# Optimization experiments

Measured on AMD Instinct MI355X. Metric: run time of the kernel, lower is better.

Reference implementation:

```python
import jax, jax.numpy as jnp
import numpy as np

H = 16          # local heads
DN = 128        # qk_nope_head_dim
DR = 64         # qk_rope_head_dim
DV = 128        # v_head_dim
QL = 1536       # q_lora_rank
KVL = 512       # kv_lora_rank
HID = 5120      # hidden_size
T = 2048        # tokens
EPS = 1e-6
THETA = 10000.0
SCALE = (DN + DR) ** -0.5


def rmsnorm(x, w):
    return x * jax.lax.rsqrt(jnp.mean(x * x, axis=-1, keepdims=True) + EPS) * w


def rope_interleaved(x, pos):
    # non-neox (GPT-J interleaved) partial RoPE on last dim DR; x: [T, h, DR]
    inv_freq = 1.0 / (THETA ** (jnp.arange(0, DR, 2, dtype=jnp.float32) / DR))
    freqs = pos[:, None].astype(jnp.float32) * inv_freq          # [T, DR/2]
    cos = jnp.cos(freqs)[:, None, :]
    sin = jnp.sin(freqs)[:, None, :]
    x1, x2 = x[..., 0::2], x[..., 1::2]
    o1 = x1 * cos - x2 * sin
    o2 = x2 * cos + x1 * sin
    return jnp.stack([o1, o2], axis=-1).reshape(x.shape)


def setup_inputs() -> dict:
    key = jax.random.key(0)
    ks = jax.random.split(key, 8)
    s = lambda d: 1.0 / np.sqrt(d)
    return {
        "positions": jnp.arange(T, dtype=jnp.int64),
        "hidden_states": jax.random.normal(ks[0], (T, HID), jnp.float32),
        "wq_a": jax.random.normal(ks[1], (HID, QL), jnp.float32) * s(HID),
        "q_a_ln": jnp.ones((QL,), jnp.float32),
        "wq_b": jax.random.normal(ks[2], (QL, H * (DN + DR)), jnp.float32) * s(QL),
        "wkv_a": jax.random.normal(ks[3], (HID, KVL + DR), jnp.float32) * s(HID),
        "kv_a_ln": jnp.ones((KVL,), jnp.float32),
        "wkv_b": jax.random.normal(ks[4], (KVL, H * (DN + DV)), jnp.float32) * s(KVL),
        "wo": jax.random.normal(ks[5], (H * DV, HID), jnp.float32) * s(H * DV),
    }


def reference(positions, hidden_states, wq_a, q_a_ln, wq_b, wkv_a, kv_a_ln, wkv_b, wo):
    Tn = hidden_states.shape[0]
    # Q path: low-rank down, RMSNorm, up to per-head qk dims
    q = rmsnorm(hidden_states @ wq_a, q_a_ln) @ wq_b            # [T, H*(DN+DR)]
    q = q.reshape(Tn, H, DN + DR)
    q_nope, q_pe = q[..., :DN], q[..., DN:]
    # KV path: joint down-projection -> latent + shared rope key
    kv = hidden_states @ wkv_a                                   # [T, KVL+DR]
    c_kv, k_pe = kv[:, :KVL], kv[:, KVL:]
    c_kv = rmsnorm(c_kv, kv_a_ln)
    kvb = (c_kv @ wkv_b).reshape(Tn, H, DN + DV)
    k_nope, v = kvb[..., :DN], kvb[..., DN:]
    # partial RoPE on rope sub-dims only
    q_pe = rope_interleaved(q_pe, positions)                     # [T, H, DR]
    k_pe = rope_interleaved(k_pe[:, None, :], positions)         # [T, 1, DR]
    # causal attention over full qk_head_dim
    scores = (jnp.einsum('thd,shd->hts', q_nope, k_nope)
              + jnp.einsum('thd,sod->hts', q_pe, k_pe)) * SCALE  # [H, T, T]
    mask = jnp.tril(jnp.ones((Tn, Tn), bool))
    scores = jnp.where(mask[None], scores, jnp.finfo(scores.dtype).min)
    attn = jax.nn.softmax(scores, axis=-1)
    out = jnp.einsum('hts,shd->thd', attn, v).reshape(Tn, H * DV)
    return out @ wo                                              # [T, HID]
```

## Files before the change

kernel.cpp:

```cpp
#include <hip/hip_runtime.h>
#include <hip/hip_bf16.h>

typedef __attribute__((ext_vector_type(8))) short bf16x8;
typedef __attribute__((ext_vector_type(4))) short bf16x4;
typedef __attribute__((ext_vector_type(4))) float f32x4;

typedef __attribute__((address_space(1))) const unsigned int gu32;
typedef __attribute__((address_space(3))) unsigned int lu32;

#define ATTN_SCALE 0.07216878364870323f

static __device__ __forceinline__ float bf2f(__hip_bfloat16 b) { return __bfloat162float(b); }

__global__ void cvt_kernel(const float* __restrict__ in, __hip_bfloat16* __restrict__ out, int n) {
  for (int i = (blockIdx.x * 256 + threadIdx.x) * 4; i < n; i += gridDim.x * 256 * 4) {
    float4 v = *(const float4*)(in + i);
    out[i + 0] = __float2bfloat16(v.x);
    out[i + 1] = __float2bfloat16(v.y);
    out[i + 2] = __float2bfloat16(v.z);
    out[i + 3] = __float2bfloat16(v.w);
  }
}

__global__ void transpose_cvt_kernel(const float* __restrict__ in, __hip_bfloat16* __restrict__ out,
                                     int R, int C) {
  __shared__ float tile[32][33];
  int bi = blockIdx.x, bj = blockIdx.y;
  int tx = threadIdx.x & 31, ty = threadIdx.x >> 5;
#pragma unroll
  for (int k2 = 0; k2 < 4; k2++) {
    int r = bi * 32 + ty + k2 * 8;
    tile[ty + k2 * 8][tx] = in[(size_t)r * C + bj * 32 + tx];
  }
  __syncthreads();
#pragma unroll
  for (int k2 = 0; k2 < 4; k2++) {
    int cc = bj * 32 + ty + k2 * 8;
    out[(size_t)cc * R + bi * 32 + tx] = __float2bfloat16(tile[tx][ty + k2 * 8]);
  }
}

__global__ void rmsnorm_kernel(const float* __restrict__ in, int in_stride, int cols,
                               const float* __restrict__ wgt,
                               __hip_bfloat16* __restrict__ out, int out_stride) {
  int row = blockIdx.x;
  const float* x = in + (size_t)row * in_stride;
  float ss = 0.f;
  for (int c = threadIdx.x; c < cols; c += 256) { float v = x[c]; ss += v * v; }
#pragma unroll
  for (int d = 1; d < 64; d <<= 1) ss += __shfl_xor(ss, d, 64);
  __shared__ float red[4];
  if ((threadIdx.x & 63) == 0) red[threadIdx.x >> 6] = ss;
  __syncthreads();
  float tot = red[0] + red[1] + red[2] + red[3];
  float r = rsqrtf(tot / cols + 1e-6f);
  __hip_bfloat16* o = out + (size_t)row * out_stride;
  for (int c = threadIdx.x; c < cols; c += 256)
    o[c] = __float2bfloat16(x[c] * r * wgt[c]);
}

__global__ void rope_q_kernel(__hip_bfloat16* __restrict__ q) {
  int row = blockIdx.x;
#pragma unroll
  for (int jj = 0; jj < 2; jj++) {
    int v = threadIdx.x + 256 * jj;
    int h = v >> 5, i = v & 31;
    float inv = powf(10000.f, -(2.f * i) / 64.f);
    float fr = (float)row * inv;
    float s, c;
    sincosf(fr, &s, &c);
    __hip_bfloat16* p = q + (size_t)row * 3072 + h * 192 + 128 + 2 * i;
    float x1 = bf2f(p[0]), x2 = bf2f(p[1]);
    p[0] = __float2bfloat16(x1 * c - x2 * s);
    p[1] = __float2bfloat16(x2 * c + x1 * s);
  }
}

__global__ void rope_k_kernel(const float* __restrict__ src, int stride,
                              __hip_bfloat16* __restrict__ kpe) {
  int row = blockIdx.x;
  int i = threadIdx.x;
  if (i < 32) {
    float inv = powf(10000.f, -(2.f * i) / 64.f);
    float fr = (float)row * inv;
    float s, c;
    sincosf(fr, &s, &c);
    float x1 = src[(size_t)row * stride + 2 * i];
    float x2 = src[(size_t)row * stride + 2 * i + 1];
    kpe[(size_t)row * 64 + 2 * i]     = __float2bfloat16(x1 * c - x2 * s);
    kpe[(size_t)row * 64 + 2 * i + 1] = __float2bfloat16(x2 * c + x1 * s);
  }
}

template <int MODE>
__global__ __launch_bounds__(256, 2) void gemm_lds_kernel(
    const __hip_bfloat16* __restrict__ A, const __hip_bfloat16* __restrict__ Bt,
    void* __restrict__ Cout, __hip_bfloat16* __restrict__ KnopeOut,
    __hip_bfloat16* __restrict__ VtOut, int M, int N, int K) {
  __shared__ __hip_bfloat16 As[2][128][32];
  __shared__ __hip_bfloat16 Bs[2][128][32];
  const int t = threadIdx.x;
  const int w = t >> 6, l = t & 63;
  const int lr = l & 15, lh = l >> 4;
  const int wr = w >> 1, wc = w & 1;
  const int bm = blockIdx.x, bn = blockIdx.y;

  const int r0 = l >> 2;
  const int c0 = (l & 3) * 8;
  const int rowA0 = w * 16 + r0;
  const int rowA1 = (4 + w) * 16 + r0;
  const __hip_bfloat16* Ag0 = A + (size_t)(bm * 128 + rowA0) * K + c0;
  const __hip_bfloat16* Ag1 = A + (size_t)(bm * 128 + rowA1) * K + c0;
  int br0 = bn * 128 + rowA0; if (br0 >= N) br0 = N - 1;
  int br1 = bn * 128 + rowA1; if (br1 >= N) br1 = N - 1;
  const __hip_bfloat16* Bg0 = Bt + (size_t)br0 * K + c0;
  const __hip_bfloat16* Bg1 = Bt + (size_t)br1 * K + c0;

  f32x4 acc[4][4];
#pragma unroll
  for (int i = 0; i < 4; i++)
#pragma unroll
    for (int j = 0; j < 4; j++) acc[i][j] = f32x4{0.f, 0.f, 0.f, 0.f};

  auto issue = [&](int kt, int buf) {
    const int ko = kt * 32;
    __builtin_amdgcn_global_load_lds((gu32*)(Ag0 + ko), (lu32*)&As[buf][rowA0][c0], 16, 0, 0);
    __builtin_amdgcn_global_load_lds((gu32*)(Ag1 + ko), (lu32*)&As[buf][rowA1][c0], 16, 0, 0);
    __builtin_amdgcn_global_load_lds((gu32*)(Bg0 + ko), (lu32*)&Bs[buf][rowA0][c0], 16, 0, 0);
    __builtin_amdgcn_global_load_lds((gu32*)(Bg1 + ko), (lu32*)&Bs[buf][rowA1][c0], 16, 0, 0);
  };

  const int KT = K >> 5;
  issue(0, 0);
  int cur = 0;
  for (int kt = 0; kt < KT; ++kt) {
    __syncthreads();
    if (kt + 1 < KT) issue(kt + 1, cur ^ 1);
    bf16x8 af[4], bff[4];
#pragma unroll
    for (int m = 0; m < 4; m++) af[m] = *(bf16x8*)&As[cur][wr * 64 + m * 16 + lr][lh * 8];
#pragma unroll
    for (int n = 0; n < 4; n++) bff[n] = *(bf16x8*)&Bs[cur][wc * 64 + n * 16 + lr][lh * 8];
    __builtin_amdgcn_s_setprio(1);
#pragma unroll
    for (int m = 0; m < 4; m++)
#pragma unroll
      for (int n = 0; n < 4; n++)
        acc[m][n] = __builtin_amdgcn_mfma_f32_16x16x32_bf16(af[m], bff[n], acc[m][n], 0, 0, 0);
    __builtin_amdgcn_s_setprio(0);
    cur ^= 1;
  }
#pragma unroll
  for (int m = 0; m < 4; m++) {
    int row = bm * 128 + wr * 64 + m * 16 + lh * 4;
#pragma unroll
    for (int n = 0; n < 4; n++) {
      int col = bn * 128 + wc * 64 + n * 16 + lr;
      if (MODE == 2) {
        int hcol = ((col >> 8) << 7) + (col & 127);
        if ((bn & 1) == 0) {
#pragma unroll
          for (int j = 0; j < 4; j++)
            KnopeOut[(size_t)(row + j) * 2048 + hcol] = __float2bfloat16(acc[m][n][j]);
        } else {
          bf16x4 pk;
#pragma unroll
          for (int j = 0; j < 4; j++) {
            union { __hip_bfloat16 b; short s; } cv;
            cv.b = __float2bfloat16(acc[m][n][j]);
            pk[j] = cv.s;
          }
          *(bf16x4*)(VtOut + (size_t)hcol * 2048 + row) = pk;
        }
      } else if (col < N) {
#pragma unroll
        for (int j = 0; j < 4; j++) {
          if (MODE == 1)
            ((__hip_bfloat16*)Cout)[(size_t)(row + j) * N + col] = __float2bfloat16(acc[m][n][j]);
          else
            ((float*)Cout)[(size_t)(row + j) * N + col] = acc[m][n][j];
        }
      }
    }
  }
}

__global__ __launch_bounds__(256, 2) void attn_kernel(
    const __hip_bfloat16* __restrict__ Q, const __hip_bfloat16* __restrict__ Knope,
    const __hip_bfloat16* __restrict__ Vt, const __hip_bfloat16* __restrict__ KPE,
    __hip_bfloat16* __restrict__ Out) {
  __shared__ __hip_bfloat16 Ks[64][200];
  __shared__ __hip_bfloat16 Vs[128][72];
  __shared__ __hip_bfloat16 Ps[4][16][72];

  const int t = threadIdx.x;
  const int w = t >> 6, l = t & 63;
  const int lr = l & 15, lh = l >> 4;
  const int bm = (int)gridDim.x - 1 - (int)blockIdx.x;
  const int h = blockIdx.y;

  bf16x8 aq[6];
  {
    const int qrow = bm * 64 + w * 16 + lr;
    const __hip_bfloat16* qp = Q + (size_t)qrow * 3072 + h * 192 + lh * 8;
#pragma unroll
    for (int ks = 0; ks < 6; ks++) aq[ks] = *(const bf16x8*)(qp + ks * 32);
  }

  f32x4 o_acc[8];
#pragma unroll
  for (int i = 0; i < 8; i++) o_acc[i] = f32x4{0.f, 0.f, 0.f, 0.f};
  float m_run[4], l_run[4];
#pragma unroll
  for (int j = 0; j < 4; j++) { m_run[j] = -INFINITY; l_run[j] = 0.f; }

  bf16x8 kreg[6], vreg[4];
  auto load_regs = [&](int kb) {
    const int s0 = kb * 64;
#pragma unroll
    for (int j = 0; j < 6; j++) {
      int c = t + 256 * j;
      int row = c / 24, col8 = (c % 24) * 8;
      const __hip_bfloat16* src = (col8 < 128)
          ? Knope + (size_t)(s0 + row) * 2048 + h * 128 + col8
          : KPE + (size_t)(s0 + row) * 64 + (col8 - 128);
      kreg[j] = *(const bf16x8*)src;
    }
#pragma unroll
    for (int j = 0; j < 4; j++) {
      int c = t + 256 * j;
      int dv = c >> 3;
      int sc = c & 7;
      vreg[j] = *(const bf16x8*)(Vt + (size_t)(h * 128 + dv) * 2048 + s0 + sc * 8);
    }
  };
  auto store_tile = [&]() {
#pragma unroll
    for (int j = 0; j < 6; j++) {
      int c = t + 256 * j;
      int row = c / 24, col8 = (c % 24) * 8;
      *(bf16x8*)&Ks[row][col8] = kreg[j];
    }
#pragma unroll
    for (int j = 0; j < 4; j++) {
      int c = t + 256 * j;
      int dv = c >> 3, sc = c & 7;
      *(bf16x8*)&Vs[dv][(sc ^ ((dv >> 3) & 7)) << 3] = vreg[j];
    }
  };

  load_regs(0);
  for (int kb = 0; kb <= bm; ++kb) {
    const int s0 = kb * 64;
    store_tile();
    __syncthreads();
    if (kb < bm) load_regs(kb + 1);

    f32x4 sa[4];
#pragma unroll
    for (int nf = 0; nf < 4; nf++) sa[nf] = f32x4{0.f, 0.f, 0.f, 0.f};
#pragma unroll
    for (int ks = 0; ks < 6; ks++) {
#pragma unroll
      for (int nf = 0; nf < 4; nf++) {
        bf16x8 b = *(bf16x8*)&Ks[nf * 16 + lr][ks * 32 + lh * 8];
        sa[nf] = __builtin_amdgcn_mfma_f32_16x16x32_bf16(aq[ks], b, sa[nf], 0, 0, 0);
      }
    }
    float sv[4][4];
    const bool diag = (kb == bm);
#pragma unroll
    for (int nf = 0; nf < 4; nf++) {
      int scol = s0 + nf * 16 + lr;
#pragma unroll
      for (int j = 0; j < 4; j++) {
        float x = sa[nf][j] * ATTN_SCALE;
        if (diag) {
          int qr = bm * 64 + w * 16 + lh * 4 + j;
          if (scol > qr) x = -1e30f;
        }
        sv[nf][j] = x;
      }
    }
    float pm[4], fac[4];
#pragma unroll
    for (int j = 0; j < 4; j++) {
      float mx = fmaxf(fmaxf(sv[0][j], sv[1][j]), fmaxf(sv[2][j], sv[3][j]));
#pragma unroll
      for (int d = 1; d < 16; d <<= 1) mx = fmaxf(mx, __shfl_xor(mx, d, 64));
      float mn = fmaxf(m_run[j], mx);
      fac[j] = __expf(m_run[j] - mn);
      m_run[j] = mn;
      pm[j] = mn;
    }
    float rs[4] = {0.f, 0.f, 0.f, 0.f};
#pragma unroll
    for (int nf = 0; nf < 4; nf++) {
#pragma unroll
      for (int j = 0; j < 4; j++) {
        float p = __expf(sv[nf][j] - pm[j]);
        rs[j] += p;
        Ps[w][lh * 4 + j][nf * 16 + lr] = __float2bfloat16(p);
      }
    }
#pragma unroll
    for (int j = 0; j < 4; j++) {
      float s = rs[j];
#pragma unroll
      for (int d = 1; d < 16; d <<= 1) s += __shfl_xor(s, d, 64);
      l_run[j] = l_run[j] * fac[j] + s;
    }
#pragma unroll
    for (int nf = 0; nf < 8; nf++)
#pragma unroll
      for (int j = 0; j < 4; j++) o_acc[nf][j] *= fac[j];

#pragma unroll
    for (int ks = 0; ks < 2; ks++) {
      bf16x8 pa = *(bf16x8*)&Ps[w][lr][ks * 32 + lh * 8];
#pragma unroll
      for (int nf = 0; nf < 8; nf++) {
        int dv = nf * 16 + lr;
        int c8 = ks * 4 + lh;
        bf16x8 vb = *(bf16x8*)&Vs[dv][((c8 ^ ((dv >> 3) & 7)) << 3)];
        o_acc[nf] = __builtin_amdgcn_mfma_f32_16x16x32_bf16(pa, vb, o_acc[nf], 0, 0, 0);
      }
    }
    __syncthreads();
  }
#pragma unroll
  for (int nf = 0; nf < 8; nf++) {
    int col = h * 128 + nf * 16 + lr;
#pragma unroll
    for (int j = 0; j < 4; j++) {
      int row = bm * 64 + w * 16 + lh * 4 + j;
      Out[(size_t)row * 2048 + col] = __float2bfloat16(o_acc[nf][j] / l_run[j]);
    }
  }
}

extern "C" void kernel_launch(void* const* d_in, const int* in_sizes, int n_in,
                              void* d_out, int out_size, void* d_ws, size_t ws_size,
                              hipStream_t stream) {
  const float* hidden  = (const float*)d_in[1];
  const float* wq_a    = (const float*)d_in[2];
  const float* q_a_ln  = (const float*)d_in[3];
  const float* wq_b    = (const float*)d_in[4];
  const float* wkv_a   = (const float*)d_in[5];
  const float* kv_a_ln = (const float*)d_in[6];
  const float* wkv_b   = (const float*)d_in[7];
  const float* wo      = (const float*)d_in[8];
  float* out = (float*)d_out;

  char* ws = (char*)d_ws;
  size_t off = 0;
  auto alloc = [&](size_t bytes) { void* p = ws + off; off += (bytes + 255) & ~(size_t)255; return p; };
  __hip_bfloat16* h_bf     = (__hip_bfloat16*)alloc((size_t)2048 * 5120 * 2);
  __hip_bfloat16* qkvw_t   = (__hip_bfloat16*)alloc((size_t)2112 * 5120 * 2);
  __hip_bfloat16* wq_b_t   = (__hip_bfloat16*)alloc((size_t)3072 * 1536 * 2);
  __hip_bfloat16* wkv_b_t  = (__hip_bfloat16*)alloc((size_t)4096 * 512 * 2);
  __hip_bfloat16* wo_t     = (__hip_bfloat16*)alloc((size_t)5120 * 2048 * 2);
  float*          qkv_lat  = (float*)alloc((size_t)2048 * 2112 * 4);
  __hip_bfloat16* q_a_bf   = (__hip_bfloat16*)alloc((size_t)2048 * 1536 * 2);
  __hip_bfloat16* ckv_bf   = (__hip_bfloat16*)alloc((size_t)2048 * 512 * 2);
  __hip_bfloat16* kpe_bf   = (__hip_bfloat16*)alloc((size_t)2048 * 64 * 2);
  __hip_bfloat16* q_bf     = (__hip_bfloat16*)alloc((size_t)2048 * 3072 * 2);
  __hip_bfloat16* knope_bf = (__hip_bfloat16*)alloc((size_t)2048 * 2048 * 2);
  __hip_bfloat16* vt_bf    = (__hip_bfloat16*)alloc((size_t)2048 * 2048 * 2);
  __hip_bfloat16* attn_o   = (__hip_bfloat16*)alloc((size_t)2048 * 2048 * 2);
  (void)ws_size; (void)in_sizes; (void)n_in; (void)out_size;

  cvt_kernel<<<1024, 256, 0, stream>>>(hidden, h_bf, 2048 * 5120);
  transpose_cvt_kernel<<<dim3(160, 48), 256, 0, stream>>>(wq_a, qkvw_t, 5120, 1536);
  transpose_cvt_kernel<<<dim3(160, 18), 256, 0, stream>>>(wkv_a, qkvw_t + (size_t)1536 * 5120, 5120, 576);
  transpose_cvt_kernel<<<dim3(48, 96), 256, 0, stream>>>(wq_b, wq_b_t, 1536, 3072);
  transpose_cvt_kernel<<<dim3(16, 128), 256, 0, stream>>>(wkv_b, wkv_b_t, 512, 4096);
  transpose_cvt_kernel<<<dim3(64, 160), 256, 0, stream>>>(wo, wo_t, 2048, 5120);

  gemm_lds_kernel<0><<<dim3(16, 17), 256, 0, stream>>>(h_bf, qkvw_t, qkv_lat, nullptr, nullptr,
                                                       2048, 2112, 5120);

  rmsnorm_kernel<<<2048, 256, 0, stream>>>(qkv_lat, 2112, 1536, q_a_ln, q_a_bf, 1536);
  rmsnorm_kernel<<<2048, 256, 0, stream>>>(qkv_lat + 1536, 2112, 512, kv_a_ln, ckv_bf, 512);
  rope_k_kernel<<<2048, 64, 0, stream>>>(qkv_lat + 2048, 2112, kpe_bf);

  gemm_lds_kernel<1><<<dim3(16, 24), 256, 0, stream>>>(q_a_bf, wq_b_t, q_bf, nullptr, nullptr,
                                                       2048, 3072, 1536);
  rope_q_kernel<<<2048, 256, 0, stream>>>(q_bf);

  gemm_lds_kernel<2><<<dim3(16, 32), 256, 0, stream>>>(ckv_bf, wkv_b_t, nullptr, knope_bf, vt_bf,
                                                       2048, 4096, 512);

  attn_kernel<<<dim3(32, 16), 256, 0, stream>>>(q_bf, knope_bf, vt_bf, kpe_bf, attn_o);

  gemm_lds_kernel<0><<<dim3(16, 40), 256, 0, stream>>>(attn_o, wo_t, out, nullptr, nullptr,
                                                       2048, 5120, 2048);
}
```

Measured before the change: 545.3 us.

## Split long causal attention rows into KV chunks with a combine kernel

The attention grid is split so that query blocks with long causal ranges process KV in chunks of 8 tiles across separate workgroups, producing 80x16 blocks instead of 32x16. Partial unnormalized outputs and running max/sum are written to a float workspace. A new combine kernel merges the partials with log-sum-exp rescaling. This aims to fix load imbalance and underuse of the GPU's compute units in causal attention, at the cost of extra global traffic for partials and one more kernel launch.

```diff
diff --git a/kernel.cpp b/kernel.cpp
--- a/kernel.cpp
+++ b/kernel.cpp
@@ -188,7 +188,7 @@
 __global__ __launch_bounds__(256, 2) void attn_kernel(
     const __hip_bfloat16* __restrict__ Q, const __hip_bfloat16* __restrict__ Knope,
     const __hip_bfloat16* __restrict__ Vt, const __hip_bfloat16* __restrict__ KPE,
-    __hip_bfloat16* __restrict__ Out) {
+    __hip_bfloat16* __restrict__ Out, float* __restrict__ Opart, float2* __restrict__ MLpart) {
   __shared__ __hip_bfloat16 Ks[64][200];
   __shared__ __hip_bfloat16 Vs[128][72];
   __shared__ __hip_bfloat16 Ps[4][16][72];
@@ -196,8 +196,18 @@
   const int t = threadIdx.x;
   const int w = t >> 6, l = t & 63;
   const int lr = l & 15, lh = l >> 4;
-  const int bm = (int)gridDim.x - 1 - (int)blockIdx.x;
   const int h = blockIdx.y;
+
+  const int x = blockIdx.x;
+  const int g = (x >= 48) ? 3 : (x >= 24) ? 2 : (x >= 8) ? 1 : 0;
+  const int Sg = (g == 3) ? 48 : (g == 2) ? 24 : (g == 1) ? 8 : 0;
+  const int r = x - Sg;
+  const int q = r / (g + 1);
+  const int bm = g * 8 + q;
+  const int ci = r - q * (g + 1);
+  const int kb0 = ci * 8;
+  const int kb_last = (bm < kb0 + 7) ? bm : kb0 + 7;
+  const bool partial = (g > 0);
 
   bf16x8 aq[6];
   {
@@ -249,12 +259,12 @@
     }
   };
 
-  load_regs(0);
-  for (int kb = 0; kb <= bm; ++kb) {
+  load_regs(kb0);
+  for (int kb = kb0; kb <= kb_last; ++kb) {
     const int s0 = kb * 64;
     store_tile();
     __syncthreads();
-    if (kb < bm) load_regs(kb + 1);
+    if (kb < kb_last) load_regs(kb + 1);
 
     f32x4 sa[4];
 #pragma unroll
@@ -274,12 +284,12 @@
       int scol = s0 + nf * 16 + lr;
 #pragma unroll
       for (int j = 0; j < 4; j++) {
-        float x = sa[nf][j] * ATTN_SCALE;
+        float xv = sa[nf][j] * ATTN_SCALE;
         if (diag) {
           int qr = bm * 64 + w * 16 + lh * 4 + j;
-          if (scol > qr) x = -1e30f;
+          if (scol > qr) xv = -1e30f;
         }
-        sv[nf][j] = x;
+        sv[nf][j] = xv;
       }
     }
     float pm[4], fac[4];
@@ -328,15 +338,78 @@
     }
     __syncthreads();
   }
-#pragma unroll
-  for (int nf = 0; nf < 8; nf++) {
-    int col = h * 128 + nf * 16 + lr;
-#pragma unroll
-    for (int j = 0; j < 4; j++) {
-      int row = bm * 64 + w * 16 + lh * 4 + j;
-      Out[(size_t)row * 2048 + col] = __float2bfloat16(o_acc[nf][j] / l_run[j]);
-    }
-  }
+
+  if (!partial) {
+#pragma unroll
+    for (int nf = 0; nf < 8; nf++) {
+      int col = h * 128 + nf * 16 + lr;
+#pragma unroll
+      for (int j = 0; j < 4; j++) {
+        int row = bm * 64 + w * 16 + lh * 4 + j;
+        Out[(size_t)row * 2048 + col] = __float2bfloat16(o_acc[nf][j] / l_run[j]);
+      }
+    }
+  } else {
+    const int base = ((g == 1) ? 0 : (g == 2) ? 16 : 40) + q * (g + 1);
+    const int slot = h * 72 + base + ci;
+    float* op = Opart + (size_t)slot * 8192;
+#pragma unroll
+    for (int nf = 0; nf < 8; nf++) {
+      int col = nf * 16 + lr;
+#pragma unroll
+      for (int j = 0; j < 4; j++) {
+        int row = w * 16 + lh * 4 + j;
+        op[row * 128 + col] = o_acc[nf][j];
+      }
+    }
+    if (lr == 0) {
+#pragma unroll
+      for (int j = 0; j < 4; j++) {
+        int row = w * 16 + lh * 4 + j;
+        MLpart[(size_t)slot * 64 + row] = float2{m_run[j], l_run[j]};
+      }
+    }
+  }
+}
+
+__global__ void attn_combine_kernel(const float* __restrict__ Opart,
+                                    const float2* __restrict__ MLpart,
+                                    __hip_bfloat16* __restrict__ Out) {
+  const int bm = 8 + blockIdx.x, h = blockIdx.y;
+  const int g = bm >> 3;
+  const int nch = g + 1;
+  const int base = ((g == 1) ? 0 : (g == 2) ? 16 : 40) + (bm & 7) * nch;
+  const int slot0 = h * 72 + base;
+  const int row = threadIdx.x >> 2;
+  const int c0 = (threadIdx.x & 3) * 32;
+
+  float M = -INFINITY;
+  for (int c = 0; c < nch; ++c) M = fmaxf(M, MLpart[(size_t)(slot0 + c) * 64 + row].x);
+  float L = 0.f;
+  for (int c = 0; c < nch; ++c) {
+    float2 ml = MLpart[(size_t)(slot0 + c) * 64 + row];
+    L += ml.y * __expf(ml.x - M);
+  }
+  float acc[32];
+#pragma unroll
+  for (int i = 0; i < 32; i++) acc[i] = 0.f;
+  for (int c = 0; c < nch; ++c) {
+    float2 ml = MLpart[(size_t)(slot0 + c) * 64 + row];
+    float sc = __expf(ml.x - M);
+    const float* op = Opart + (size_t)(slot0 + c) * 8192 + row * 128 + c0;
+#pragma unroll
+    for (int k = 0; k < 8; k++) {
+      float4 v = *(const float4*)(op + k * 4);
+      acc[k * 4 + 0] += sc * v.x;
+      acc[k * 4 + 1] += sc * v.y;
+      acc[k * 4 + 2] += sc * v.z;
+      acc[k * 4 + 3] += sc * v.w;
+    }
+  }
+  const float inv = 1.f / L;
+  __hip_bfloat16* o = Out + (size_t)(bm * 64 + row) * 2048 + h * 128 + c0;
+#pragma unroll
+  for (int i = 0; i < 32; i++) o[i] = __float2bfloat16(acc[i] * inv);
 }
 
 extern "C" void kernel_launch(void* const* d_in, const int* in_sizes, int n_in,
@@ -368,6 +441,8 @@
   __hip_bfloat16* knope_bf = (__hip_bfloat16*)alloc((size_t)2048 * 2048 * 2);
   __hip_bfloat16* vt_bf    = (__hip_bfloat16*)alloc((size_t)2048 * 2048 * 2);
   __hip_bfloat16* attn_o   = (__hip_bfloat16*)alloc((size_t)2048 * 2048 * 2);
+  float*          opart    = (float*)alloc((size_t)1152 * 8192 * 4);
+  float2*         mlpart   = (float2*)alloc((size_t)1152 * 64 * 8);
   (void)ws_size; (void)in_sizes; (void)n_in; (void)out_size;
 
   cvt_kernel<<<1024, 256, 0, stream>>>(hidden, h_bf, 2048 * 5120);
@@ -391,7 +466,9 @@
   gemm_lds_kernel<2><<<dim3(16, 32), 256, 0, stream>>>(ckv_bf, wkv_b_t, nullptr, knope_bf, vt_bf,
                                                        2048, 4096, 512);
 
-  attn_kernel<<<dim3(32, 16), 256, 0, stream>>>(q_bf, knope_bf, vt_bf, kpe_bf, attn_o);
+  attn_kernel<<<dim3(80, 16), 256, 0, stream>>>(q_bf, knope_bf, vt_bf, kpe_bf, attn_o,
+                                                opart, mlpart);
+  attn_combine_kernel<<<dim3(24, 16), 256, 0, stream>>>(opart, mlpart, attn_o);
 
   gemm_lds_kernel<0><<<dim3(16, 40), 256, 0, stream>>>(attn_o, wo_t, out, nullptr, nullptr,
                                                        2048, 5120, 2048);
```

Result: faster. 522.4 us (-4.2%).
